# Kernel optimization log

Measured on AMD Instinct MI355X. Metric: run time of the kernel, lower is better.

## Reference

```python
import jax, jax.numpy as jnp
import numpy as np
from jax import lax

NUM_HEADS = 8
NUM_SELECTS = 10
CLIP = 10.0  # tanh logit clipping in pointer-style SingleHeadAttention
NEG = -1e9   # finite -inf substitute (safe under autodiff)


def setup_inputs() -> dict:
    key = jax.random.key(0)
    ks = jax.random.split(key, 8)
    B, N, D = 64, 2048, 256
    s = 1.0 / np.sqrt(D)
    return {
        "encoder_output": jax.random.normal(ks[0], (B, N, D), jnp.float32),
        "in_proj_w": jax.random.uniform(ks[1], (3 * D, D), jnp.float32, -s, s),
        "in_proj_b": jnp.zeros((3 * D,), jnp.float32),
        "out_w": jax.random.uniform(ks[2], (D, D), jnp.float32, -s, s),
        "out_b": jnp.zeros((D,), jnp.float32),
        "sha_wq": jax.random.uniform(ks[3], (D, D), jnp.float32, -s, s),
        "sha_wk": jax.random.uniform(ks[4], (D, D), jnp.float32, -s, s),
        "is_training": False,
    }


def reference(encoder_output, in_proj_w, in_proj_b, out_w, out_b, sha_wq, sha_wk, is_training):
    B, N, D = encoder_output.shape
    H, dh, S = NUM_HEADS, D // NUM_HEADS, NUM_SELECTS
    Wq, Wk, Wv = in_proj_w[:D], in_proj_w[D:2 * D], in_proj_w[2 * D:]
    bq, bk, bv = in_proj_b[:D], in_proj_b[D:2 * D], in_proj_b[2 * D:]

    h_mean = jnp.mean(encoder_output, axis=1)                         # [B,D]
    # MHA query is constant across steps; K/V projections of the encoder too.
    q = (h_mean @ Wq.T + bq).reshape(B, H, dh)                        # [B,H,dh]
    k = (encoder_output @ Wk.T + bk).reshape(B, N, H, dh)             # [B,N,H,dh]
    v = (encoder_output @ Wv.T + bv).reshape(B, N, H, dh)             # [B,N,H,dh]
    ksingle = encoder_output @ sha_wk.T                               # [B,N,D]
    scale = 1.0 / np.sqrt(dh)
    scale2 = 1.0 / np.sqrt(D)
    bidx = jnp.arange(B)

    def step(mask, _):
        # multi-head cross attention, key_padding_mask = mask
        s_mha = jnp.einsum('bhd,bnhd->bhn', q, k) * scale             # [B,H,N]
        s_mha = jnp.where(mask[:, None, :], NEG, s_mha)
        a = jax.nn.softmax(s_mha, axis=-1)
        ctx = jnp.einsum('bhn,bnhd->bhd', a, v).reshape(B, D)
        attn_out = ctx @ out_w.T + out_b                              # [B,D]
        # single-head pointer attention with tanh clipping
        qs = attn_out @ sha_wq.T                                      # [B,D]
        u = CLIP * jnp.tanh(jnp.einsum('bd,bnd->bn', qs, ksingle) * scale2)
        u = jnp.where(mask, NEG, u)                                   # [B,N]
        logp = jax.nn.log_softmax(u, axis=-1)
        p = jnp.exp(logp)
        ent = -jnp.sum(jnp.where(p > 0, p * logp, 0.0), axis=-1)
        # is_training=False path: greedy argmax (deterministic reference)
        idx = jnp.argmax(p, axis=-1)                                  # [B]
        pi_s = p[bidx, idx]
        new_mask = mask.at[bidx, idx].set(True)
        return new_mask, (idx, pi_s, ent)

    mask0 = jnp.zeros((B, N), dtype=bool)
    _, (idxs, pis, ents) = lax.scan(step, mask0, None, length=S)
    selected_clients = idxs.T.astype(jnp.int64 if jax.config.jax_enable_x64 else jnp.int32)  # [B,S]
    pi = pis.T                                                        # [B,S]
    entropy = jnp.sum(ents, axis=0)                                   # [B]
    return selected_clients, pi, entropy
```

## Files before the change

kernel.cpp:

```cpp
#include <hip/hip_runtime.h>
#include <hip/hip_bf16.h>
#include <math.h>

namespace {
constexpr int Bc = 64, Nc = 2048, Dc = 256, Hc = 8, DHc = 32, Sc = 10;
constexpr float kNeg = -1000000000.0f;
constexpr float kClip = 10.0f;
constexpr float kScale = 0.17677669529663687f;
constexpr float kScale2 = 0.0625f;
}

__global__ __launch_bounds__(256) void k_hmean_part(const float* __restrict__ enc,
                                                    float* __restrict__ hpart) {
  int b = blockIdx.x >> 3, c = blockIdx.x & 7, d = threadIdx.x;
  const float* p = enc + ((size_t)b * Nc + c * 256) * Dc + d;
  float s = 0.f;
  for (int n = 0; n < 256; ++n) s += p[(size_t)n * Dc];
  hpart[(size_t)blockIdx.x * Dc + d] = s;
}

__global__ __launch_bounds__(256) void k_hmean_red(const float* __restrict__ hpart,
                                                   float* __restrict__ hmean) {
  int b = blockIdx.x, d = threadIdx.x;
  float s = 0.f;
  for (int c = 0; c < 8; ++c) s += hpart[(size_t)(b * 8 + c) * Dc + d];
  hmean[b * Dc + d] = s * (1.0f / Nc);
}

__global__ __launch_bounds__(256) void k_qgc(const float* __restrict__ hmean,
                                             const float* __restrict__ w_in,
                                             const float* __restrict__ b_in,
                                             float* __restrict__ g, float* __restrict__ c) {
  int b = blockIdx.x, t = threadIdx.x;
  __shared__ float hm[Dc];
  __shared__ float qsh[Dc];
  hm[t] = hmean[b * Dc + t];
  __syncthreads();
  {
    const float* row = w_in + (size_t)t * Dc;
    float acc = b_in[t];
    for (int d = 0; d < Dc; ++d) acc += row[d] * hm[d];
    qsh[t] = acc;
  }
  __syncthreads();
  for (int h = 0; h < Hc; ++h) {
    float acc = 0.f;
    const float* wk = w_in + (size_t)(Dc + h * DHc) * Dc + t;
    const float* qh = qsh + h * DHc;
    #pragma unroll 8
    for (int i = 0; i < DHc; ++i) acc += qh[i] * wk[(size_t)i * Dc];
    g[((size_t)b * Hc + h) * Dc + t] = acc;
  }
  if (t < Hc) {
    float acc = 0.f;
    for (int i = 0; i < DHc; ++i) acc += qsh[t * DHc + i] * b_in[Dc + t * DHc + i];
    c[b * Hc + t] = acc;
  }
}

__global__ __launch_bounds__(256) void k_A1(const float* __restrict__ swq,
                                            const float* __restrict__ ow,
                                            const float* __restrict__ ob,
                                            float* __restrict__ M1, float* __restrict__ m1b) {
  int i = blockIdx.x, e = threadIdx.x;
  __shared__ float row[Dc];
  __shared__ float red[256];
  row[e] = swq[(size_t)i * Dc + e];
  __syncthreads();
  float acc = 0.f;
  #pragma unroll 4
  for (int k = 0; k < Dc; ++k) acc += row[k] * ow[(size_t)k * Dc + e];
  M1[(size_t)i * Dc + e] = acc;
  red[e] = row[e] * ob[e];
  __syncthreads();
  for (int off = 128; off >= 1; off >>= 1) {
    if (e < off) red[e] += red[e + off];
    __syncthreads();
  }
  if (e == 0) m1b[i] = red[0];
}

__global__ __launch_bounds__(256) void k_A2(const float* __restrict__ swk,
                                            const float* __restrict__ M1,
                                            const float* __restrict__ m1b,
                                            const float* __restrict__ b_in,
                                            float* __restrict__ Aout, float* __restrict__ cvec) {
  int d = blockIdx.x, e = threadIdx.x;
  __shared__ float col[Dc];
  __shared__ float red[256];
  col[e] = swk[(size_t)e * Dc + d];
  __syncthreads();
  float acc = 0.f;
  #pragma unroll 4
  for (int k = 0; k < Dc; ++k) acc += col[k] * M1[(size_t)k * Dc + e];
  Aout[(size_t)d * Dc + e] = acc;
  red[e] = acc * b_in[2 * Dc + e] + col[e] * m1b[e];
  __syncthreads();
  for (int off = 128; off >= 1; off >>= 1) {
    if (e < off) red[e] += red[e + off];
    __syncthreads();
  }
  if (e == 0) cvec[d] = red[0];
}

__global__ __launch_bounds__(256) void k_A3(const float* __restrict__ Aout,
                                            const float* __restrict__ w_in,
                                            float* __restrict__ BT) {
  int h = blockIdx.x >> 3, et = blockIdx.x & 7, d = threadIdx.x;
  float arow[DHc];
  #pragma unroll
  for (int i = 0; i < DHc; ++i) arow[i] = Aout[(size_t)d * Dc + h * DHc + i];
  __shared__ float wv[DHc][DHc];
  for (int k = threadIdx.x; k < DHc * DHc; k += 256) {
    int i = k >> 5, j = k & 31;
    wv[i][j] = w_in[(size_t)(2 * Dc + h * DHc + i) * Dc + et * DHc + j];
  }
  __syncthreads();
  for (int j = 0; j < DHc; ++j) {
    float acc = 0.f;
    #pragma unroll
    for (int i = 0; i < DHc; ++i) acc += arow[i] * wv[i][j];
    BT[((size_t)h * Dc + et * DHc + j) * Dc + d] = acc;
  }
}

__global__ __launch_bounds__(256) void k_scores(const float* __restrict__ enc,
                                                const float* __restrict__ g,
                                                const float* __restrict__ c,
                                                float* __restrict__ s) {
  int b = blockIdx.x >> 3, nt = blockIdx.x & 7, t = threadIdx.x;
  int n0 = nt * 256;
  __shared__ float gsm[Hc * Dc];
  __shared__ float csm[Hc];
  __shared__ float el[256 * 33];
  for (int k = t; k < Hc * Dc; k += 256) gsm[k] = g[(size_t)b * Hc * Dc + k];
  if (t < Hc) csm[t] = c[b * Hc + t];
  int row = t >> 3, d4 = t & 7;
  const float* src = enc + ((size_t)b * Nc + n0) * Dc;
  float4 v[8];
  #pragma unroll
  for (int p = 0; p < 8; ++p)
    v[p] = *reinterpret_cast<const float4*>(src + (size_t)(p * 32 + row) * Dc + d4 * 4);
  float acc[Hc] = {};
  for (int ch = 0; ch < 8; ++ch) {
    __syncthreads();
    #pragma unroll
    for (int p = 0; p < 8; ++p) {
      float* dst = &el[(p * 32 + row) * 33 + d4 * 4];
      dst[0] = v[p].x; dst[1] = v[p].y; dst[2] = v[p].z; dst[3] = v[p].w;
    }
    __syncthreads();
    if (ch < 7) {
      #pragma unroll
      for (int p = 0; p < 8; ++p)
        v[p] = *reinterpret_cast<const float4*>(src + (size_t)(p * 32 + row) * Dc + (ch + 1) * 32 + d4 * 4);
    }
    const float* gb = gsm + ch * 32;
    #pragma unroll
    for (int q = 0; q < 8; ++q) {
      float e0 = el[t * 33 + q * 4 + 0];
      float e1 = el[t * 33 + q * 4 + 1];
      float e2 = el[t * 33 + q * 4 + 2];
      float e3 = el[t * 33 + q * 4 + 3];
      #pragma unroll
      for (int h = 0; h < Hc; ++h) {
        const float4 g4 = *reinterpret_cast<const float4*>(gb + h * Dc + q * 4);
        acc[h] += e0 * g4.x + e1 * g4.y + e2 * g4.z + e3 * g4.w;
      }
    }
  }
  #pragma unroll
  for (int h = 0; h < Hc; ++h)
    s[((size_t)b * Hc + h) * Nc + n0 + t] = kScale * (acc[h] + csm[h]);
}

__global__ __launch_bounds__(256) void k_smax(const float* __restrict__ s,
                                              float* __restrict__ w, float* __restrict__ W0) {
  int bh = blockIdx.x, t = threadIdx.x;
  __shared__ float red[256];
  float lv[8];
  float m = -3.0e38f;
  #pragma unroll
  for (int q = 0; q < 8; ++q) {
    lv[q] = s[(size_t)bh * Nc + q * 256 + t];
    m = fmaxf(m, lv[q]);
  }
  red[t] = m;
  __syncthreads();
  for (int off = 128; off >= 1; off >>= 1) {
    if (t < off) red[t] = fmaxf(red[t], red[t + off]);
    __syncthreads();
  }
  m = red[0];
  __syncthreads();
  float ssum = 0.f;
  #pragma unroll
  for (int q = 0; q < 8; ++q) {
    float e = expf(lv[q] - m);
    w[(size_t)bh * Nc + q * 256 + t] = e;
    ssum += e;
  }
  red[t] = ssum;
  __syncthreads();
  for (int off = 128; off >= 1; off >>= 1) {
    if (t < off) red[t] += red[t + off];
    __syncthreads();
  }
  if (t == 0) W0[bh] = red[0];
}

__global__ __launch_bounds__(256) void k_S0part(const float* __restrict__ enc,
                                                const float* __restrict__ w,
                                                float* __restrict__ Spart) {
  int b = blockIdx.x >> 3, cid = blockIdx.x & 7, t = threadIdx.x;
  __shared__ float wsm[Hc * 256];
  for (int k = t; k < Hc * 256; k += 256) {
    int h = k >> 8, ni = k & 255;
    wsm[k] = w[((size_t)b * Hc + h) * Nc + cid * 256 + ni];
  }
  __syncthreads();
  float acc[Hc] = {};
  const float* ep = enc + ((size_t)b * Nc + cid * 256) * Dc + t;
  for (int ni = 0; ni < 256; ++ni) {
    float ev = ep[(size_t)ni * Dc];
    #pragma unroll
    for (int h = 0; h < Hc; ++h) acc[h] += wsm[h * 256 + ni] * ev;
  }
  #pragma unroll
  for (int h = 0; h < Hc; ++h)
    Spart[(((size_t)b * 8 + cid) * Hc + h) * Dc + t] = acc[h];
}

__global__ __launch_bounds__(256) void k_S0red(const float* __restrict__ Spart,
                                               float* __restrict__ Sacc) {
  int b = blockIdx.x >> 3, h = blockIdx.x & 7, t = threadIdx.x;
  float acc = 0.f;
  for (int cid = 0; cid < 8; ++cid)
    acc += Spart[(((size_t)b * 8 + cid) * Hc + h) * Dc + t];
  Sacc[((size_t)b * Hc + h) * Dc + t] = acc;
}

__global__ __launch_bounds__(256) void k_chain(const float* __restrict__ Sacc,
                                               const float* __restrict__ W0,
                                               const float* __restrict__ w,
                                               const float* __restrict__ enc,
                                               const int* __restrict__ hist,
                                               const float* __restrict__ BT,
                                               float* __restrict__ rpart, int tstep) {
  int b = blockIdx.x >> 3, h = blockIdx.x & 7, t = threadIdx.x;
  __shared__ float sh[Dc];
  float se = Sacc[((size_t)b * Hc + h) * Dc + t];
  float Wh = W0[b * Hc + h];
  for (int tt = 0; tt < tstep; ++tt) {
    int j = hist[b * 16 + tt];
    float wv = w[((size_t)b * Hc + h) * Nc + j];
    se -= wv * enc[((size_t)b * Nc + j) * Dc + t];
    Wh -= wv;
  }
  sh[t] = se / Wh;
  __syncthreads();
  float acc = 0.f;
  const float* bt = BT + (size_t)h * Dc * Dc + t;
  #pragma unroll 8
  for (int e = 0; e < Dc; ++e) acc += bt[(size_t)e * Dc] * sh[e];
  rpart[((size_t)b * Hc + h) * Dc + t] = acc;
}

__global__ __launch_bounds__(256) void k_uscore(const float* __restrict__ enc,
                                                const float* __restrict__ rpart,
                                                const float* __restrict__ cvec,
                                                float* __restrict__ u) {
  int b = blockIdx.x >> 3, nt = blockIdx.x & 7, t = threadIdx.x;
  int n0 = nt * 256;
  __shared__ float rsm[Dc];
  __shared__ float el[256 * 33];
  {
    float vsum = cvec[t];
    #pragma unroll
    for (int h = 0; h < Hc; ++h) vsum += rpart[((size_t)b * Hc + h) * Dc + t];
    rsm[t] = vsum;
  }
  int row = t >> 3, d4 = t & 7;
  const float* src = enc + ((size_t)b * Nc + n0) * Dc;
  float4 v[8];
  #pragma unroll
  for (int p = 0; p < 8; ++p)
    v[p] = *reinterpret_cast<const float4*>(src + (size_t)(p * 32 + row) * Dc + d4 * 4);
  float acc = 0.f;
  for (int ch = 0; ch < 8; ++ch) {
    __syncthreads();
    #pragma unroll
    for (int p = 0; p < 8; ++p) {
      float* dst = &el[(p * 32 + row) * 33 + d4 * 4];
      dst[0] = v[p].x; dst[1] = v[p].y; dst[2] = v[p].z; dst[3] = v[p].w;
    }
    __syncthreads();
    if (ch < 7) {
      #pragma unroll
      for (int p = 0; p < 8; ++p)
        v[p] = *reinterpret_cast<const float4*>(src + (size_t)(p * 32 + row) * Dc + (ch + 1) * 32 + d4 * 4);
    }
    const float* rb = rsm + ch * 32;
    #pragma unroll
    for (int q = 0; q < 8; ++q) {
      const float4 r4 = *reinterpret_cast<const float4*>(rb + q * 4);
      acc += el[t * 33 + q * 4 + 0] * r4.x + el[t * 33 + q * 4 + 1] * r4.y +
             el[t * 33 + q * 4 + 2] * r4.z + el[t * 33 + q * 4 + 3] * r4.w;
    }
  }
  u[(size_t)b * Nc + n0 + t] = kClip * tanhf(kScale2 * acc);
}

__global__ __launch_bounds__(256) void k_select(const float* __restrict__ u,
                                                int* __restrict__ mask, int* __restrict__ hist,
                                                float* __restrict__ out, int tstep) {
  int b = blockIdx.x, t = threadIdx.x;
  __shared__ float red[256];
  __shared__ int redi[256];
  float uval[8];
  float lmax = -3.0e38f;
  int lidx = 0;
  #pragma unroll
  for (int q = 0; q < 8; ++q) {
    int n = t + q * 256;
    float v = u[(size_t)b * Nc + n];
    if (mask[b * Nc + n]) v = kNeg;
    uval[q] = v;
    if (v > lmax) { lmax = v; lidx = n; }
  }
  red[t] = lmax; redi[t] = lidx;
  __syncthreads();
  for (int off = 128; off >= 1; off >>= 1) {
    if (t < off) {
      float o = red[t + off]; int oi = redi[t + off];
      if (o > red[t] || (o == red[t] && oi < redi[t])) { red[t] = o; redi[t] = oi; }
    }
    __syncthreads();
  }
  float mu = red[0];
  int gidx = redi[0];
  __syncthreads();
  float ssum = 0.f;
  #pragma unroll
  for (int q = 0; q < 8; ++q) ssum += expf(uval[q] - mu);
  red[t] = ssum;
  __syncthreads();
  for (int off = 128; off >= 1; off >>= 1) {
    if (t < off) red[t] += red[t + off];
    __syncthreads();
  }
  float Z = red[0];
  float lse = mu + logf(Z);
  __syncthreads();
  float ent = 0.f;
  #pragma unroll
  for (int q = 0; q < 8; ++q) {
    float logp = uval[q] - lse;
    float p = expf(logp);
    if (p > 0.f) ent -= p * logp;
  }
  red[t] = ent;
  __syncthreads();
  for (int off = 128; off >= 1; off >>= 1) {
    if (t < off) red[t] += red[t + off];
    __syncthreads();
  }
  if (t == 0) {
    float enttot = red[0];
    float pi = expf(u[(size_t)b * Nc + gidx] - lse);
    out[b * Sc + tstep] = (float)gidx;
    out[Bc * Sc + b * Sc + tstep] = pi;
    if (tstep == 0) out[2 * Bc * Sc + b] = enttot;
    else out[2 * Bc * Sc + b] += enttot;
    hist[b * 16 + tstep] = gidx;
    mask[b * Nc + gidx] = 1;
  }
}

extern "C" void kernel_launch(void* const* d_in, const int* in_sizes, int n_in,
                              void* d_out, int out_size, void* d_ws, size_t ws_size,
                              hipStream_t stream) {
  (void)in_sizes; (void)n_in; (void)out_size; (void)ws_size;
  const float* enc  = (const float*)d_in[0];
  const float* in_w = (const float*)d_in[1];
  const float* in_b = (const float*)d_in[2];
  const float* ow   = (const float*)d_in[3];
  const float* ob   = (const float*)d_in[4];
  const float* swq  = (const float*)d_in[5];
  const float* swk  = (const float*)d_in[6];
  float* out = (float*)d_out;

  float* ws = (float*)d_ws;
  size_t off = 0;
  auto alloc = [&](size_t n) { float* p = ws + off; off += n; return p; };
  float* hpart = alloc((size_t)Bc * 8 * Dc);
  float* hmean = alloc((size_t)Bc * Dc);
  float* g     = alloc((size_t)Bc * Hc * Dc);
  float* c     = alloc((size_t)Bc * Hc);
  float* s     = alloc((size_t)Bc * Hc * Nc);
  float* w     = alloc((size_t)Bc * Hc * Nc);
  float* W0    = alloc((size_t)Bc * Hc);
  float* Spart = alloc((size_t)Bc * 8 * Hc * Dc);
  float* Sacc  = alloc((size_t)Bc * Hc * Dc);
  float* M1    = alloc((size_t)Dc * Dc);
  float* m1b   = alloc(Dc);
  float* Aout  = alloc((size_t)Dc * Dc);
  float* cvec  = alloc(Dc);
  float* BT    = alloc((size_t)Hc * Dc * Dc);
  float* rpart = alloc((size_t)Bc * Hc * Dc);
  float* u     = alloc((size_t)Bc * Nc);
  int* mask    = (int*)alloc((size_t)Bc * Nc);
  int* hist    = (int*)alloc((size_t)Bc * 16);

  k_hmean_part<<<Bc * 8, 256, 0, stream>>>(enc, hpart);
  k_hmean_red<<<Bc, 256, 0, stream>>>(hpart, hmean);
  k_qgc<<<Bc, 256, 0, stream>>>(hmean, in_w, in_b, g, c);
  k_A1<<<Dc, 256, 0, stream>>>(swq, ow, ob, M1, m1b);
  k_A2<<<Dc, 256, 0, stream>>>(swk, M1, m1b, in_b, Aout, cvec);
  k_A3<<<Hc * 8, 256, 0, stream>>>(Aout, in_w, BT);
  k_scores<<<Bc * 8, 256, 0, stream>>>(enc, g, c, s);
  k_smax<<<Bc * Hc, 256, 0, stream>>>(s, w, W0);
  k_S0part<<<Bc * 8, 256, 0, stream>>>(enc, w, Spart);
  k_S0red<<<Bc * Hc, 256, 0, stream>>>(Spart, Sacc);
  hipMemsetAsync(mask, 0, (size_t)Bc * Nc * sizeof(int), stream);

  for (int t = 0; t < Sc; ++t) {
    k_chain<<<Bc * Hc, 256, 0, stream>>>(Sacc, W0, w, enc, hist, BT, rpart, t);
    k_uscore<<<Bc * 8, 256, 0, stream>>>(enc, rpart, cvec, u);
    k_select<<<Bc, 256, 0, stream>>>(u, mask, hist, out, t);
  }
}
```

Before: 548.0 us.

## Fuse selection into chain kernel and read encoder rows directly in score kernels

The per-step select kernel is merged into a single per-batch chain kernel that first runs the previous step's selection and then computes the reduced query vector, including the head sum and cvec that k_uscore used to do. This cuts the per-step launches from three to two, with a final select launch after the loop. The score and u-score kernels drop the LDS transpose staging and have each thread read its own encoder row as float4. That avoids syncs and LDS traffic but makes the global loads strided per thread, and the chain kernel now runs only 64 blocks, each doing an 8x larger BT matvec.

```diff
diff --git a/kernel.cpp b/kernel.cpp
--- a/kernel.cpp
+++ b/kernel.cpp
@@ -129,49 +129,26 @@
                                                 const float* __restrict__ c,
                                                 float* __restrict__ s) {
   int b = blockIdx.x >> 3, nt = blockIdx.x & 7, t = threadIdx.x;
-  int n0 = nt * 256;
+  int n = nt * 256 + t;
   __shared__ float gsm[Hc * Dc];
   __shared__ float csm[Hc];
-  __shared__ float el[256 * 33];
   for (int k = t; k < Hc * Dc; k += 256) gsm[k] = g[(size_t)b * Hc * Dc + k];
   if (t < Hc) csm[t] = c[b * Hc + t];
-  int row = t >> 3, d4 = t & 7;
-  const float* src = enc + ((size_t)b * Nc + n0) * Dc;
-  float4 v[8];
-  #pragma unroll
-  for (int p = 0; p < 8; ++p)
-    v[p] = *reinterpret_cast<const float4*>(src + (size_t)(p * 32 + row) * Dc + d4 * 4);
+  __syncthreads();
+  const float4* row = reinterpret_cast<const float4*>(enc + ((size_t)b * Nc + n) * Dc);
   float acc[Hc] = {};
-  for (int ch = 0; ch < 8; ++ch) {
-    __syncthreads();
-    #pragma unroll
-    for (int p = 0; p < 8; ++p) {
-      float* dst = &el[(p * 32 + row) * 33 + d4 * 4];
-      dst[0] = v[p].x; dst[1] = v[p].y; dst[2] = v[p].z; dst[3] = v[p].w;
-    }
-    __syncthreads();
-    if (ch < 7) {
-      #pragma unroll
-      for (int p = 0; p < 8; ++p)
-        v[p] = *reinterpret_cast<const float4*>(src + (size_t)(p * 32 + row) * Dc + (ch + 1) * 32 + d4 * 4);
-    }
-    const float* gb = gsm + ch * 32;
-    #pragma unroll
-    for (int q = 0; q < 8; ++q) {
-      float e0 = el[t * 33 + q * 4 + 0];
-      float e1 = el[t * 33 + q * 4 + 1];
-      float e2 = el[t * 33 + q * 4 + 2];
-      float e3 = el[t * 33 + q * 4 + 3];
-      #pragma unroll
-      for (int h = 0; h < Hc; ++h) {
-        const float4 g4 = *reinterpret_cast<const float4*>(gb + h * Dc + q * 4);
-        acc[h] += e0 * g4.x + e1 * g4.y + e2 * g4.z + e3 * g4.w;
-      }
+  #pragma unroll 8
+  for (int d4 = 0; d4 < 64; ++d4) {
+    const float4 e = row[d4];
+    #pragma unroll
+    for (int h = 0; h < Hc; ++h) {
+      const float4 g4 = *reinterpret_cast<const float4*>(gsm + h * Dc + d4 * 4);
+      acc[h] += e.x * g4.x + e.y * g4.y + e.z * g4.z + e.w * g4.w;
     }
   }
   #pragma unroll
   for (int h = 0; h < Hc; ++h)
-    s[((size_t)b * Hc + h) * Nc + n0 + t] = kScale * (acc[h] + csm[h]);
+    s[((size_t)b * Hc + h) * Nc + n] = kScale * (acc[h] + csm[h]);
 }
 
 __global__ __launch_bounds__(256) void k_smax(const float* __restrict__ s,
@@ -240,80 +217,130 @@
   Sacc[((size_t)b * Hc + h) * Dc + t] = acc;
 }
 
-__global__ __launch_bounds__(256) void k_chain(const float* __restrict__ Sacc,
-                                               const float* __restrict__ W0,
-                                               const float* __restrict__ w,
-                                               const float* __restrict__ enc,
-                                               const int* __restrict__ hist,
-                                               const float* __restrict__ BT,
-                                               float* __restrict__ rpart, int tstep) {
-  int b = blockIdx.x >> 3, h = blockIdx.x & 7, t = threadIdx.x;
-  __shared__ float sh[Dc];
-  float se = Sacc[((size_t)b * Hc + h) * Dc + t];
-  float Wh = W0[b * Hc + h];
-  for (int tt = 0; tt < tstep; ++tt) {
-    int j = hist[b * 16 + tt];
-    float wv = w[((size_t)b * Hc + h) * Nc + j];
-    se -= wv * enc[((size_t)b * Nc + j) * Dc + t];
-    Wh -= wv;
-  }
-  sh[t] = se / Wh;
-  __syncthreads();
-  float acc = 0.f;
-  const float* bt = BT + (size_t)h * Dc * Dc + t;
+__global__ __launch_bounds__(256) void k_selchain(const float* __restrict__ u,
+                                                  int* __restrict__ mask, int* __restrict__ hist,
+                                                  float* __restrict__ out,
+                                                  const float* __restrict__ Sacc,
+                                                  const float* __restrict__ W0,
+                                                  const float* __restrict__ w,
+                                                  const float* __restrict__ enc,
+                                                  const float* __restrict__ BT,
+                                                  const float* __restrict__ cvec,
+                                                  float* __restrict__ r, int tstep) {
+  int b = blockIdx.x, t = threadIdx.x;
+  __shared__ float sh[Hc * Dc];
+  __shared__ float red[256];
+  __shared__ int redi[256];
+  __shared__ int histsh[16];
+  if (t < 16) histsh[t] = hist[b * 16 + t];
+  __syncthreads();
+
+  if (tstep > 0) {
+    int sel_t = tstep - 1;
+    float uval[8];
+    float lmax = -3.0e38f;
+    int lidx = 0;
+    #pragma unroll
+    for (int q = 0; q < 8; ++q) {
+      int n = t + q * 256;
+      float v = u[(size_t)b * Nc + n];
+      if (mask[b * Nc + n]) v = kNeg;
+      uval[q] = v;
+      if (v > lmax) { lmax = v; lidx = n; }
+    }
+    red[t] = lmax; redi[t] = lidx;
+    __syncthreads();
+    for (int off = 128; off >= 1; off >>= 1) {
+      if (t < off) {
+        float o = red[t + off]; int oi = redi[t + off];
+        if (o > red[t] || (o == red[t] && oi < redi[t])) { red[t] = o; redi[t] = oi; }
+      }
+      __syncthreads();
+    }
+    float mu = red[0];
+    int gidx = redi[0];
+    __syncthreads();
+    float ssum = 0.f;
+    #pragma unroll
+    for (int q = 0; q < 8; ++q) ssum += expf(uval[q] - mu);
+    red[t] = ssum;
+    __syncthreads();
+    for (int off = 128; off >= 1; off >>= 1) {
+      if (t < off) red[t] += red[t + off];
+      __syncthreads();
+    }
+    float Z = red[0];
+    float lse = mu + logf(Z);
+    __syncthreads();
+    float ent = 0.f;
+    #pragma unroll
+    for (int q = 0; q < 8; ++q) {
+      float logp = uval[q] - lse;
+      float p = expf(logp);
+      if (p > 0.f) ent -= p * logp;
+    }
+    red[t] = ent;
+    __syncthreads();
+    for (int off = 128; off >= 1; off >>= 1) {
+      if (t < off) red[t] += red[t + off];
+      __syncthreads();
+    }
+    if (t == 0) {
+      float enttot = red[0];
+      float pi = expf(u[(size_t)b * Nc + gidx] - lse);
+      out[b * Sc + sel_t] = (float)gidx;
+      out[Bc * Sc + b * Sc + sel_t] = pi;
+      if (sel_t == 0) out[2 * Bc * Sc + b] = enttot;
+      else out[2 * Bc * Sc + b] += enttot;
+      hist[b * 16 + sel_t] = gidx;
+      histsh[sel_t] = gidx;
+      mask[b * Nc + gidx] = 1;
+    }
+    __syncthreads();
+  }
+
+  #pragma unroll
+  for (int h = 0; h < Hc; ++h) {
+    float se = Sacc[((size_t)b * Hc + h) * Dc + t];
+    float Wh = W0[b * Hc + h];
+    for (int tt = 0; tt < tstep; ++tt) {
+      int j = histsh[tt];
+      float wv = w[((size_t)b * Hc + h) * Nc + j];
+      se -= wv * enc[((size_t)b * Nc + j) * Dc + t];
+      Wh -= wv;
+    }
+    sh[h * Dc + t] = se / Wh;
+  }
+  __syncthreads();
+  float acc = cvec[t];
+  const float* bt = BT + t;
   #pragma unroll 8
-  for (int e = 0; e < Dc; ++e) acc += bt[(size_t)e * Dc] * sh[e];
-  rpart[((size_t)b * Hc + h) * Dc + t] = acc;
+  for (int k = 0; k < Hc * Dc; ++k) acc += bt[(size_t)k * Dc] * sh[k];
+  r[b * Dc + t] = acc;
 }
 
 __global__ __launch_bounds__(256) void k_uscore(const float* __restrict__ enc,
-                                                const float* __restrict__ rpart,
-                                                const float* __restrict__ cvec,
+                                                const float* __restrict__ r,
                                                 float* __restrict__ u) {
   int b = blockIdx.x >> 3, nt = blockIdx.x & 7, t = threadIdx.x;
-  int n0 = nt * 256;
-  __shared__ float rsm[Dc];
-  __shared__ float el[256 * 33];
-  {
-    float vsum = cvec[t];
-    #pragma unroll
-    for (int h = 0; h < Hc; ++h) vsum += rpart[((size_t)b * Hc + h) * Dc + t];
-    rsm[t] = vsum;
-  }
-  int row = t >> 3, d4 = t & 7;
-  const float* src = enc + ((size_t)b * Nc + n0) * Dc;
-  float4 v[8];
-  #pragma unroll
-  for (int p = 0; p < 8; ++p)
-    v[p] = *reinterpret_cast<const float4*>(src + (size_t)(p * 32 + row) * Dc + d4 * 4);
+  int n = nt * 256 + t;
+  __shared__ __align__(16) float rsm[Dc];
+  rsm[t] = r[b * Dc + t];
+  __syncthreads();
+  const float4* row = reinterpret_cast<const float4*>(enc + ((size_t)b * Nc + n) * Dc);
   float acc = 0.f;
-  for (int ch = 0; ch < 8; ++ch) {
-    __syncthreads();
-    #pragma unroll
-    for (int p = 0; p < 8; ++p) {
-      float* dst = &el[(p * 32 + row) * 33 + d4 * 4];
-      dst[0] = v[p].x; dst[1] = v[p].y; dst[2] = v[p].z; dst[3] = v[p].w;
-    }
-    __syncthreads();
-    if (ch < 7) {
-      #pragma unroll
-      for (int p = 0; p < 8; ++p)
-        v[p] = *reinterpret_cast<const float4*>(src + (size_t)(p * 32 + row) * Dc + (ch + 1) * 32 + d4 * 4);
-    }
-    const float* rb = rsm + ch * 32;
-    #pragma unroll
-    for (int q = 0; q < 8; ++q) {
-      const float4 r4 = *reinterpret_cast<const float4*>(rb + q * 4);
-      acc += el[t * 33 + q * 4 + 0] * r4.x + el[t * 33 + q * 4 + 1] * r4.y +
-             el[t * 33 + q * 4 + 2] * r4.z + el[t * 33 + q * 4 + 3] * r4.w;
-    }
-  }
-  u[(size_t)b * Nc + n0 + t] = kClip * tanhf(kScale2 * acc);
-}
-
-__global__ __launch_bounds__(256) void k_select(const float* __restrict__ u,
-                                                int* __restrict__ mask, int* __restrict__ hist,
-                                                float* __restrict__ out, int tstep) {
+  #pragma unroll 16
+  for (int d4 = 0; d4 < 64; ++d4) {
+    const float4 e = row[d4];
+    const float4 rr = *reinterpret_cast<const float4*>(rsm + d4 * 4);
+    acc += e.x * rr.x + e.y * rr.y + e.z * rr.z + e.w * rr.w;
+  }
+  u[(size_t)b * Nc + n] = kClip * tanhf(kScale2 * acc);
+}
+
+__global__ __launch_bounds__(256) void k_selfinal(const float* __restrict__ u,
+                                                  int* __restrict__ mask,
+                                                  float* __restrict__ out) {
   int b = blockIdx.x, t = threadIdx.x;
   __shared__ float red[256];
   __shared__ int redi[256];
@@ -368,12 +395,9 @@
   if (t == 0) {
     float enttot = red[0];
     float pi = expf(u[(size_t)b * Nc + gidx] - lse);
-    out[b * Sc + tstep] = (float)gidx;
-    out[Bc * Sc + b * Sc + tstep] = pi;
-    if (tstep == 0) out[2 * Bc * Sc + b] = enttot;
-    else out[2 * Bc * Sc + b] += enttot;
-    hist[b * 16 + tstep] = gidx;
-    mask[b * Nc + gidx] = 1;
+    out[b * Sc + (Sc - 1)] = (float)gidx;
+    out[Bc * Sc + b * Sc + (Sc - 1)] = pi;
+    out[2 * Bc * Sc + b] += enttot;
   }
 }
 
@@ -407,7 +431,7 @@
   float* Aout  = alloc((size_t)Dc * Dc);
   float* cvec  = alloc(Dc);
   float* BT    = alloc((size_t)Hc * Dc * Dc);
-  float* rpart = alloc((size_t)Bc * Hc * Dc);
+  float* r     = alloc((size_t)Bc * Dc);
   float* u     = alloc((size_t)Bc * Nc);
   int* mask    = (int*)alloc((size_t)Bc * Nc);
   int* hist    = (int*)alloc((size_t)Bc * 16);
@@ -425,8 +449,8 @@
   hipMemsetAsync(mask, 0, (size_t)Bc * Nc * sizeof(int), stream);
 
   for (int t = 0; t < Sc; ++t) {
-    k_chain<<<Bc * Hc, 256, 0, stream>>>(Sacc, W0, w, enc, hist, BT, rpart, t);
-    k_uscore<<<Bc * 8, 256, 0, stream>>>(enc, rpart, cvec, u);
-    k_select<<<Bc, 256, 0, stream>>>(u, mask, hist, out, t);
-  }
-}
+    k_selchain<<<Bc, 256, 0, stream>>>(u, mask, hist, out, Sacc, W0, w, enc, BT, cvec, r, t);
+    k_uscore<<<Bc * 8, 256, 0, stream>>>(enc, r, u);
+  }
+  k_selfinal<<<Bc, 256, 0, stream>>>(u, mask, out);
+}
```

Result: slower. 1.373 ms (+150.5%).
